# Kernel optimization log

Measured on AMD Instinct MI355X. Metric: run time of the kernel, lower is better.

## Reference

```python
import jax, jax.numpy as jnp
import numpy as np

B, N = 4, 2048

def setup_inputs() -> dict:
    key = jax.random.key(0)
    k1, k2, k3, k4 = jax.random.split(key, 4)
    return {
        "xyz": jax.random.normal(k1, (B, N, 3), dtype=jnp.float32),
        "scales": jax.random.uniform(k2, (B, N, 3), dtype=jnp.float32),
        "rotations": jax.random.normal(k3, (B, N, 4), dtype=jnp.float32),
        "velocities": jax.random.normal(k4, (B, N, 3), dtype=jnp.float32),
    }

def _quat_to_rotmat(q):
    # q: (B, N, 4) -> (B, N, 3, 3), same formula as the torch module (no normalization)
    qw, qx, qy, qz = q[..., 0], q[..., 1], q[..., 2], q[..., 3]
    R = jnp.stack([
        1 - 2 * qy**2 - 2 * qz**2, 2 * qx * qy - 2 * qz * qw, 2 * qx * qz + 2 * qy * qw,
        2 * qx * qy + 2 * qz * qw, 1 - 2 * qx**2 - 2 * qz**2, 2 * qy * qz - 2 * qx * qw,
        2 * qx * qz - 2 * qy * qw, 2 * qy * qz + 2 * qx * qw, 1 - 2 * qx**2 - 2 * qy**2,
    ], axis=-1)
    return R.reshape(q.shape[0], q.shape[1], 3, 3)

def reference(xyz, scales, rotations, velocities):
    b, n, _ = xyz.shape
    diff = xyz[:, :, None, :] - xyz[:, None, :, :]          # (B,N,N,3)
    dist = jnp.sqrt(jnp.sum(diff * diff, axis=-1) + 1e-8)    # (B,N,N)
    direction = diff / dist[..., None]                        # (B,N,N,3)

    R = _quat_to_rotmat(rotations)                            # (B,N,3,3)
    u_R = jnp.einsum('bnmi,bnij->bnmj', direction, R)         # (B,N,N,3)
    u_R_S = u_R * scales[:, None, :, :]                       # scale of gaussian m
    r_directional = jnp.sqrt(jnp.sum(u_R_S * u_R_S, axis=-1))  # (B,N,N)
    r_total = r_directional + jnp.swapaxes(r_directional, 1, 2)

    overlap = jax.nn.relu(r_total - dist)                     # (B,N,N)
    spectral_repulsion = overlap**2 / (1 + 0.1 * overlap)

    v_rel = velocities[:, :, None, :] - velocities[:, None, :, :]
    v_approach = jnp.sum(v_rel * direction, axis=-1)          # (B,N,N)
    mskd_loss = jnp.sum(overlap * jax.nn.relu(-v_approach)) / (b * n * n)

    mask = jnp.eye(n, dtype=bool)[None]                       # zero self-pairs
    spectral_repulsion = jnp.where(mask, 0.0, spectral_repulsion)
    return jnp.mean(spectral_repulsion) + 0.1 * mskd_loss
```

## Files before the change

kernel.cpp:

```cpp
#include <hip/hip_runtime.h>

#define BB 4
#define NN 2048
#define TM 64
#define SPLITM (NN / TM)
#define ROWS 2
#define BLK 256
#define RN (ROWS * BLK)
#define NGX ((NN / RN) * SPLITM)
#define NBLOCKS (NGX * BB)
#define INV_TOTAL (1.0f / ((float)BB * (float)NN * (float)NN))

__device__ __forceinline__ void quat_to_R(float qw, float qx, float qy, float qz, float* R) {
    R[0] = 1.f - 2.f * (qy * qy + qz * qz);
    R[1] = 2.f * (qx * qy - qz * qw);
    R[2] = 2.f * (qx * qz + qy * qw);
    R[3] = 2.f * (qx * qy + qz * qw);
    R[4] = 1.f - 2.f * (qx * qx + qz * qz);
    R[5] = 2.f * (qy * qz - qx * qw);
    R[6] = 2.f * (qx * qz - qy * qw);
    R[7] = 2.f * (qy * qz + qx * qw);
    R[8] = 1.f - 2.f * (qx * qx + qy * qy);
}

template <bool ATOMIC>
__global__ __launch_bounds__(BLK) void pair_kernel(
    const float* __restrict__ xyz, const float* __restrict__ scales,
    const float* __restrict__ rot, const float* __restrict__ vel,
    float* __restrict__ partials, float* __restrict__ outp)
{
    __shared__ float smx[TM], smy[TM], smz[TM];
    __shared__ float ssx[TM], ssy[TM], ssz[TM];
    __shared__ float svx[TM], svy[TM], svz[TM];
    __shared__ float sR[9][TM];

    const int tid = threadIdx.x;
    const int b   = blockIdx.y;
    const int nb  = blockIdx.x / SPLITM;
    const int ms  = blockIdx.x % SPLITM;
    const int m0  = ms * TM;

    if (tid < TM) {
        const int m = m0 + tid;
        const size_t b3 = ((size_t)b * NN + m) * 3;
        const size_t b4 = ((size_t)b * NN + m) * 4;
        smx[tid] = xyz[b3 + 0]; smy[tid] = xyz[b3 + 1]; smz[tid] = xyz[b3 + 2];
        ssx[tid] = scales[b3 + 0]; ssy[tid] = scales[b3 + 1]; ssz[tid] = scales[b3 + 2];
        svx[tid] = vel[b3 + 0]; svy[tid] = vel[b3 + 1]; svz[tid] = vel[b3 + 2];
        const float4 q = *reinterpret_cast<const float4*>(rot + b4);
        float R[9];
        quat_to_R(q.x, q.y, q.z, q.w, R);
        #pragma unroll
        for (int k = 0; k < 9; ++k) sR[k][tid] = R[k];
    }

    float px[ROWS], py[ROWS], pz[ROWS];
    float sx[ROWS], sy[ROWS], sz[ROWS];
    float vx[ROWS], vy[ROWS], vz[ROWS];
    float Rn[ROWS][9];
    #pragma unroll
    for (int r = 0; r < ROWS; ++r) {
        const int n = nb * RN + r * BLK + tid;
        const size_t b3 = ((size_t)b * NN + n) * 3;
        const size_t b4 = ((size_t)b * NN + n) * 4;
        px[r] = xyz[b3 + 0]; py[r] = xyz[b3 + 1]; pz[r] = xyz[b3 + 2];
        sx[r] = scales[b3 + 0]; sy[r] = scales[b3 + 1]; sz[r] = scales[b3 + 2];
        vx[r] = vel[b3 + 0]; vy[r] = vel[b3 + 1]; vz[r] = vel[b3 + 2];
        const float4 q = *reinterpret_cast<const float4*>(rot + b4);
        quat_to_R(q.x, q.y, q.z, q.w, Rn[r]);
    }

    __syncthreads();

    float acc = 0.f;
    #pragma unroll 4
    for (int j = 0; j < TM; ++j) {
        const float mx = smx[j], my = smy[j], mz = smz[j];
        const float msx = ssx[j], msy = ssy[j], msz = ssz[j];
        const float mvx = svx[j], mvy = svy[j], mvz = svz[j];
        const float Rm0 = sR[0][j], Rm1 = sR[1][j], Rm2 = sR[2][j];
        const float Rm3 = sR[3][j], Rm4 = sR[4][j], Rm5 = sR[5][j];
        const float Rm6 = sR[6][j], Rm7 = sR[7][j], Rm8 = sR[8][j];
        #pragma unroll
        for (int r = 0; r < ROWS; ++r) {
            const float dx = px[r] - mx, dy = py[r] - my, dz = pz[r] - mz;
            const float d2 = fmaf(dx, dx, fmaf(dy, dy, fmaf(dz, dz, 1e-8f)));
            const float rinv = __builtin_amdgcn_rsqf(d2);
            const float a0 = fmaf(dx, Rn[r][0], fmaf(dy, Rn[r][3], dz * Rn[r][6])) * msx;
            const float a1 = fmaf(dx, Rn[r][1], fmaf(dy, Rn[r][4], dz * Rn[r][7])) * msy;
            const float a2 = fmaf(dx, Rn[r][2], fmaf(dy, Rn[r][5], dz * Rn[r][8])) * msz;
            const float qa = __builtin_amdgcn_sqrtf(fmaf(a0, a0, fmaf(a1, a1, a2 * a2)));
            const float b0 = fmaf(dx, Rm0, fmaf(dy, Rm3, dz * Rm6)) * sx[r];
            const float b1 = fmaf(dx, Rm1, fmaf(dy, Rm4, dz * Rm7)) * sy[r];
            const float b2 = fmaf(dx, Rm2, fmaf(dy, Rm5, dz * Rm8)) * sz[r];
            const float qb = __builtin_amdgcn_sqrtf(fmaf(b0, b0, fmaf(b1, b1, b2 * b2)));
            const float w  = fmaxf(qa + qb - d2, 0.f);
            const float ov = w * rinv;
            const float spec = ov * ov * __builtin_amdgcn_rcpf(fmaf(0.1f, ov, 1.f));
            const float vdot = fmaf(vx[r] - mvx, dx, fmaf(vy[r] - mvy, dy, (vz[r] - mvz) * dz));
            const float ramp = fmaxf(-vdot * rinv, 0.f);
            acc += fmaf(0.1f * ov, ramp, spec);
        }
    }

    __shared__ float red[BLK];
    red[tid] = acc;
    __syncthreads();
    #pragma unroll
    for (int s = BLK / 2; s > 0; s >>= 1) {
        if (tid < s) red[tid] += red[tid + s];
        __syncthreads();
    }
    if (tid == 0) {
        if (ATOMIC) {
            atomicAdd(outp, red[0] * INV_TOTAL);
        } else {
            partials[blockIdx.y * gridDim.x + blockIdx.x] = red[0];
        }
    }
}

__global__ __launch_bounds__(BLK) void reduce_kernel(const float* __restrict__ partials,
                                                     float* __restrict__ out)
{
    __shared__ float red[BLK];
    const int tid = threadIdx.x;
    float a = 0.f;
    for (int i = tid; i < NBLOCKS; i += BLK) a += partials[i];
    red[tid] = a;
    __syncthreads();
    #pragma unroll
    for (int s = BLK / 2; s > 0; s >>= 1) {
        if (tid < s) red[tid] += red[tid + s];
        __syncthreads();
    }
    if (tid == 0) out[0] = red[0] * INV_TOTAL;
}

extern "C" void kernel_launch(void* const* d_in, const int* in_sizes, int n_in,
                              void* d_out, int out_size, void* d_ws, size_t ws_size,
                              hipStream_t stream)
{
    const float* xyz    = (const float*)d_in[0];
    const float* scales = (const float*)d_in[1];
    const float* rot    = (const float*)d_in[2];
    const float* vel    = (const float*)d_in[3];
    float* out = (float*)d_out;

    dim3 grid(NGX, BB);
    if (ws_size >= NBLOCKS * sizeof(float)) {
        float* partials = (float*)d_ws;
        pair_kernel<false><<<grid, BLK, 0, stream>>>(xyz, scales, rot, vel, partials, out);
        reduce_kernel<<<1, BLK, 0, stream>>>(partials, out);
    } else {
        hipMemsetAsync(d_out, 0, sizeof(float), stream);
        pair_kernel<true><<<grid, BLK, 0, stream>>>(xyz, scales, rot, vel, nullptr, out);
    }
}
```

Baseline: 36.87 us.

## Exploit pair symmetry with triangular tiling and fuse final reduction via last-block

```diff
diff --git a/kernel.cpp b/kernel.cpp
--- a/kernel.cpp
+++ b/kernel.cpp
@@ -2,13 +2,15 @@
 
 #define BB 4
 #define NN 2048
-#define TM 64
-#define SPLITM (NN / TM)
+#define TS 128
+#define T_TILES (NN / TS)
+#define NPAIRS (T_TILES * (T_TILES + 1) / 2)
+#define MQ 4
+#define MSTEP (TS / MQ)
+#define JOBS_PER_B (NPAIRS * MQ)
+#define NJOBS (JOBS_PER_B * BB)
+#define BLK 64
 #define ROWS 2
-#define BLK 256
-#define RN (ROWS * BLK)
-#define NGX ((NN / RN) * SPLITM)
-#define NBLOCKS (NGX * BB)
 #define INV_TOTAL (1.0f / ((float)BB * (float)NN * (float)NN))
 
 __device__ __forceinline__ void quat_to_R(float qw, float qx, float qy, float qz, float* R) {
@@ -27,46 +29,55 @@
 __global__ __launch_bounds__(BLK) void pair_kernel(
     const float* __restrict__ xyz, const float* __restrict__ scales,
     const float* __restrict__ rot, const float* __restrict__ vel,
-    float* __restrict__ partials, float* __restrict__ outp)
+    float* __restrict__ partials, unsigned int* __restrict__ counter,
+    float* __restrict__ outp)
 {
-    __shared__ float smx[TM], smy[TM], smz[TM];
-    __shared__ float ssx[TM], ssy[TM], ssz[TM];
-    __shared__ float svx[TM], svy[TM], svz[TM];
-    __shared__ float sR[9][TM];
+    __shared__ float4 sm[MSTEP][5];
 
-    const int tid = threadIdx.x;
-    const int b   = blockIdx.y;
-    const int nb  = blockIdx.x / SPLITM;
-    const int ms  = blockIdx.x % SPLITM;
-    const int m0  = ms * TM;
+    const int lane = threadIdx.x;
+    const int jid  = blockIdx.x;
+    const int b    = jid / JOBS_PER_B;
+    const int rem  = jid % JOBS_PER_B;
+    const int p    = rem >> 2;
+    const int mq   = rem & 3;
 
-    if (tid < TM) {
-        const int m = m0 + tid;
-        const size_t b3 = ((size_t)b * NN + m) * 3;
-        const size_t b4 = ((size_t)b * NN + m) * 4;
-        smx[tid] = xyz[b3 + 0]; smy[tid] = xyz[b3 + 1]; smz[tid] = xyz[b3 + 2];
-        ssx[tid] = scales[b3 + 0]; ssy[tid] = scales[b3 + 1]; ssz[tid] = scales[b3 + 2];
-        svx[tid] = vel[b3 + 0]; svy[tid] = vel[b3 + 1]; svz[tid] = vel[b3 + 2];
-        const float4 q = *reinterpret_cast<const float4*>(rot + b4);
+    int ti = (int)((sqrtf(8.f * (float)p + 1.f) - 1.f) * 0.5f);
+    while ((ti + 1) * (ti + 2) / 2 <= p) ++ti;
+    while (ti * (ti + 1) / 2 > p) --ti;
+    const int tj = p - ti * (ti + 1) / 2;
+
+    const int n_base = ti * TS;
+    const int m_base = tj * TS + mq * MSTEP;
+
+    if (lane < MSTEP) {
+        const int m = m_base + lane;
+        const size_t i3 = ((size_t)b * NN + m) * 3;
+        const size_t i4 = ((size_t)b * NN + m) * 4;
+        const float4 q = *reinterpret_cast<const float4*>(rot + i4);
         float R[9];
         quat_to_R(q.x, q.y, q.z, q.w, R);
-        #pragma unroll
-        for (int k = 0; k < 9; ++k) sR[k][tid] = R[k];
+        sm[lane][0] = make_float4(xyz[i3], xyz[i3 + 1], xyz[i3 + 2], scales[i3]);
+        sm[lane][1] = make_float4(scales[i3 + 1], scales[i3 + 2], vel[i3], vel[i3 + 1]);
+        sm[lane][2] = make_float4(vel[i3 + 2], R[0], R[1], R[2]);
+        sm[lane][3] = make_float4(R[3], R[4], R[5], R[6]);
+        sm[lane][4] = make_float4(R[7], R[8], 0.f, 0.f);
     }
 
     float px[ROWS], py[ROWS], pz[ROWS];
     float sx[ROWS], sy[ROWS], sz[ROWS];
     float vx[ROWS], vy[ROWS], vz[ROWS];
     float Rn[ROWS][9];
+    int   nidx[ROWS];
     #pragma unroll
     for (int r = 0; r < ROWS; ++r) {
-        const int n = nb * RN + r * BLK + tid;
-        const size_t b3 = ((size_t)b * NN + n) * 3;
-        const size_t b4 = ((size_t)b * NN + n) * 4;
-        px[r] = xyz[b3 + 0]; py[r] = xyz[b3 + 1]; pz[r] = xyz[b3 + 2];
-        sx[r] = scales[b3 + 0]; sy[r] = scales[b3 + 1]; sz[r] = scales[b3 + 2];
-        vx[r] = vel[b3 + 0]; vy[r] = vel[b3 + 1]; vz[r] = vel[b3 + 2];
-        const float4 q = *reinterpret_cast<const float4*>(rot + b4);
+        const int n = n_base + r * BLK + lane;
+        nidx[r] = n;
+        const size_t i3 = ((size_t)b * NN + n) * 3;
+        const size_t i4 = ((size_t)b * NN + n) * 4;
+        px[r] = xyz[i3]; py[r] = xyz[i3 + 1]; pz[r] = xyz[i3 + 2];
+        sx[r] = scales[i3]; sy[r] = scales[i3 + 1]; sz[r] = scales[i3 + 2];
+        vx[r] = vel[i3]; vy[r] = vel[i3 + 1]; vz[r] = vel[i3 + 2];
+        const float4 q = *reinterpret_cast<const float4*>(rot + i4);
         quat_to_R(q.x, q.y, q.z, q.w, Rn[r]);
     }
 
@@ -74,13 +85,19 @@
 
     float acc = 0.f;
     #pragma unroll 4
-    for (int j = 0; j < TM; ++j) {
-        const float mx = smx[j], my = smy[j], mz = smz[j];
-        const float msx = ssx[j], msy = ssy[j], msz = ssz[j];
-        const float mvx = svx[j], mvy = svy[j], mvz = svz[j];
-        const float Rm0 = sR[0][j], Rm1 = sR[1][j], Rm2 = sR[2][j];
-        const float Rm3 = sR[3][j], Rm4 = sR[4][j], Rm5 = sR[5][j];
-        const float Rm6 = sR[6][j], Rm7 = sR[7][j], Rm8 = sR[8][j];
+    for (int j = 0; j < MSTEP; ++j) {
+        const int m = m_base + j;
+        const float4 c0 = sm[j][0];
+        const float4 c1 = sm[j][1];
+        const float4 c2 = sm[j][2];
+        const float4 c3 = sm[j][3];
+        const float4 c4 = sm[j][4];
+        const float mx = c0.x, my = c0.y, mz = c0.z;
+        const float msx = c0.w, msy = c1.x, msz = c1.y;
+        const float mvx = c1.z, mvy = c1.w, mvz = c2.x;
+        const float Rm0 = c2.y, Rm1 = c2.z, Rm2 = c2.w;
+        const float Rm3 = c3.x, Rm4 = c3.y, Rm5 = c3.z;
+        const float Rm6 = c3.w, Rm7 = c4.x, Rm8 = c4.y;
         #pragma unroll
         for (int r = 0; r < ROWS; ++r) {
             const float dx = px[r] - mx, dy = py[r] - my, dz = pz[r] - mz;
@@ -96,45 +113,45 @@
             const float qb = __builtin_amdgcn_sqrtf(fmaf(b0, b0, fmaf(b1, b1, b2 * b2)));
             const float w  = fmaxf(qa + qb - d2, 0.f);
             const float ov = w * rinv;
-            const float spec = ov * ov * __builtin_amdgcn_rcpf(fmaf(0.1f, ov, 1.f));
+            const float rc = __builtin_amdgcn_rcpf(fmaf(0.1f, ov, 1.f));
             const float vdot = fmaf(vx[r] - mvx, dx, fmaf(vy[r] - mvy, dy, (vz[r] - mvz) * dz));
             const float ramp = fmaxf(-vdot * rinv, 0.f);
-            acc += fmaf(0.1f * ov, ramp, spec);
+            const float t = ov * fmaf(ov, rc, 0.1f * ramp);
+            const float wgt = (m < nidx[r]) ? 2.f : 0.f;
+            acc = fmaf(wgt, t, acc);
         }
     }
 
-    __shared__ float red[BLK];
-    red[tid] = acc;
-    __syncthreads();
     #pragma unroll
-    for (int s = BLK / 2; s > 0; s >>= 1) {
-        if (tid < s) red[tid] += red[tid + s];
-        __syncthreads();
+    for (int off = 32; off > 0; off >>= 1)
+        acc += __shfl_down(acc, off, 64);
+
+    if (ATOMIC) {
+        if (lane == 0) atomicAdd(outp, acc * INV_TOTAL);
+        return;
     }
-    if (tid == 0) {
-        if (ATOMIC) {
-            atomicAdd(outp, red[0] * INV_TOTAL);
-        } else {
-            partials[blockIdx.y * gridDim.x + blockIdx.x] = red[0];
+
+    int last = 0;
+    if (lane == 0) {
+        partials[jid] = acc;
+        __threadfence();
+        const unsigned int done = atomicAdd(counter, 1u);
+        last = (done == (unsigned int)(NJOBS - 1));
+    }
+    last = __shfl(last, 0, 64);
+    if (last) {
+        __threadfence();
+        const float4* p4 = reinterpret_cast<const float4*>(partials);
+        float s = 0.f;
+        for (int i = lane; i < NJOBS / 4; i += BLK) {
+            const float4 v = p4[i];
+            s += v.x + v.y + v.z + v.w;
         }
+        #pragma unroll
+        for (int off = 32; off > 0; off >>= 1)
+            s += __shfl_down(s, off, 64);
+        if (lane == 0) outp[0] = s * INV_TOTAL;
     }
-}
-
-__global__ __launch_bounds__(BLK) void reduce_kernel(const float* __restrict__ partials,
-                                                     float* __restrict__ out)
-{
-    __shared__ float red[BLK];
-    const int tid = threadIdx.x;
-    float a = 0.f;
-    for (int i = tid; i < NBLOCKS; i += BLK) a += partials[i];
-    red[tid] = a;
-    __syncthreads();
-    #pragma unroll
-    for (int s = BLK / 2; s > 0; s >>= 1) {
-        if (tid < s) red[tid] += red[tid + s];
-        __syncthreads();
-    }
-    if (tid == 0) out[0] = red[0] * INV_TOTAL;
 }
 
 extern "C" void kernel_launch(void* const* d_in, const int* in_sizes, int n_in,
@@ -147,13 +164,15 @@
     const float* vel    = (const float*)d_in[3];
     float* out = (float*)d_out;
 
-    dim3 grid(NGX, BB);
-    if (ws_size >= NBLOCKS * sizeof(float)) {
-        float* partials = (float*)d_ws;
-        pair_kernel<false><<<grid, BLK, 0, stream>>>(xyz, scales, rot, vel, partials, out);
-        reduce_kernel<<<1, BLK, 0, stream>>>(partials, out);
+    if (ws_size >= 256 + NJOBS * sizeof(float)) {
+        unsigned int* counter = (unsigned int*)d_ws;
+        float* partials = (float*)((char*)d_ws + 256);
+        hipMemsetAsync(counter, 0, sizeof(unsigned int), stream);
+        pair_kernel<false><<<NJOBS, BLK, 0, stream>>>(xyz, scales, rot, vel,
+                                                      partials, counter, out);
     } else {
         hipMemsetAsync(d_out, 0, sizeof(float), stream);
-        pair_kernel<true><<<grid, BLK, 0, stream>>>(xyz, scales, rot, vel, nullptr, out);
+        pair_kernel<true><<<NJOBS, BLK, 0, stream>>>(xyz, scales, rot, vel,
+                                                     nullptr, nullptr, out);
     }
 }
```

Result: slower. 62.39 us (+69.2%).
